# Performance work log

Measured on AMD Instinct MI355X. Metric: run time of the kernel, lower is better.

The kernel has to match this reference:

```python
import jax, jax.numpy as jnp
import numpy as np

EPS = 1e-8  # F.cosine_similarity eps
K = 2       # prompt_length


def setup_inputs() -> dict:
    key = jax.random.key(0)
    k1, k2, k3, k4 = jax.random.split(key, 4)
    B, DIM, NP, D = 32, 64, 4, 1024   # P: [batch, dim, N_p, D]; D == V (rows of stored table)
    E, VC = 768, 32000                 # stored table [V=D, E]; f_e: E -> vocab_dim=VC
    P = jax.random.normal(k1, (B, DIM, NP, D), dtype=jnp.float32)
    we_stored = jax.random.normal(k2, (D, E), dtype=jnp.float32) * 0.02
    fe_w = jax.random.normal(k3, (VC, E), dtype=jnp.float32) * 0.02
    fe_b = jax.random.normal(k4, (VC,), dtype=jnp.float32) * 0.02
    return {"P": P, "we_stored": we_stored, "fe_w": fe_w, "fe_b": fe_b}


def reference(P, we_stored, fe_w, fe_b):
    # word_embeddings = f_e(stored).t()  ->  [vocab_dim, V] == [VC, D]
    T = (we_stored @ fe_w.T + fe_b).T            # [VC, D]
    B, DIM, NP, D = P.shape
    # Cosine sim of each tiled embedding row (repeated N_p times) vs flattened P_i:
    #   dot(tiled_w, P_flat) = w . sum_j P[..., j, :]
    #   ||tiled_w|| = sqrt(N_p) * ||w||
    s = P.sum(axis=2)                                             # [B, DIM, D]
    w_norm = jnp.maximum(jnp.sqrt(jnp.float32(NP)) * jnp.linalg.norm(T, axis=1), EPS)   # [VC]
    p_norm = jnp.maximum(jnp.linalg.norm(P.reshape(B, DIM, -1), axis=-1), EPS)          # [B, DIM]
    scores = jnp.einsum('bdk,vk->bdv', s, T) / (w_norm[None, None, :] * p_norm[..., None])  # [B, DIM, VC]
    values, indices = jax.lax.top_k(scores, K)                    # [B, DIM, K]
    e_k = T[indices]                                              # [B, DIM, K, D]
    Z = jnp.concatenate([e_k, P], axis=2)                         # [B, DIM, NP+K, D]
    return Z, values
```

## Files before the change

### kernel.cpp

```cpp
#include <hip/hip_runtime.h>
#include <hip/hip_bf16.h>
#include <math.h>

#define B_    32
#define DIM_  64
#define NP_   4
#define D_    1024
#define E_    768
#define VC_   32000
#define R_    2048
#define KTOP  2
#define EPS_  1e-8f
#define NCB   250
#define NCAND 8

#define T_OFF    ((size_t)0)
#define TL_OFF   T_OFF
#define S_OFF    (T_OFF + (size_t)VC_ * D_)
#define INVW_OFF (S_OFF + (size_t)R_ * D_)
#define INVP_OFF (INVW_OFF + VC_)
#define WSQ_OFF  (INVP_OFF + R_)
#define PV_OFF   (WSQ_OFF + VC_)
#define PI_OFF   (PV_OFF + (size_t)R_ * NCB * 2)
#define SB_OFF   (PI_OFF + (size_t)R_ * NCB * 2)
#define TB_OFF   (SB_OFF + (size_t)R_ * D_ / 2)
#define WH_OFF   (TB_OFF + (size_t)VC_ * D_ / 2)
#define WL_OFF   (WH_OFF + (size_t)D_ * E_ / 2)
#define CAND_OFF (WL_OFF + (size_t)D_ * E_ / 2)
#define TIDX_OFF (CAND_OFF + (size_t)R_ * NCAND)
#define AH_OFF   (TIDX_OFF + (size_t)R_ * 2)
#define AL_OFF   (AH_OFF + (size_t)VC_ * E_ / 2)

#define NEG_INF (-3.4e38f)

typedef __bf16 bf16x8 __attribute__((ext_vector_type(8)));
typedef unsigned short u16x8 __attribute__((ext_vector_type(8)));
typedef float  f32x4  __attribute__((ext_vector_type(4)));

__device__ __forceinline__ void async_ld16(const void* gptr, void* lptr) {
    __builtin_amdgcn_global_load_lds(
        (const __attribute__((address_space(1))) void*)(uintptr_t)gptr,
        (__attribute__((address_space(3))) void*)(unsigned)(uintptr_t)lptr,
        16, 0, 0);
}

__device__ __forceinline__ bool better(float v, int i, float bv, int bi) {
    return (v > bv) || (v == bv && i < bi);
}

__device__ __forceinline__ float bfpair(unsigned short h, unsigned short l) {
    return __uint_as_float((unsigned)h << 16) + __uint_as_float((unsigned)l << 16);
}

__global__ __launch_bounds__(256) void k_prep_we(const float* __restrict__ x,
                                                 unsigned short* __restrict__ hi,
                                                 unsigned short* __restrict__ lo,
                                                 float* __restrict__ wsq) {
    int gi = blockIdx.x * 256 + threadIdx.x;
    if (gi < VC_) wsq[gi] = 0.f;
    int i = gi * 4;
    float4 v = *(const float4*)(x + i);
    ushort4 h, l;
    __bf16 b;
    b = (__bf16)v.x; h.x = __builtin_bit_cast(unsigned short, b); l.x = __builtin_bit_cast(unsigned short, (__bf16)(v.x - (float)b));
    b = (__bf16)v.y; h.y = __builtin_bit_cast(unsigned short, b); l.y = __builtin_bit_cast(unsigned short, (__bf16)(v.y - (float)b));
    b = (__bf16)v.z; h.z = __builtin_bit_cast(unsigned short, b); l.z = __builtin_bit_cast(unsigned short, (__bf16)(v.z - (float)b));
    b = (__bf16)v.w; h.w = __builtin_bit_cast(unsigned short, b); l.w = __builtin_bit_cast(unsigned short, (__bf16)(v.w - (float)b));
    *(ushort4*)(hi + i) = h;
    *(ushort4*)(lo + i) = l;
}

__global__ __launch_bounds__(256) void k_split(const float* __restrict__ x,
                                               unsigned short* __restrict__ hi,
                                               unsigned short* __restrict__ lo) {
    int i = (blockIdx.x * 256 + threadIdx.x) * 4;
    float4 v = *(const float4*)(x + i);
    ushort4 h, l;
    __bf16 b;
    b = (__bf16)v.x; h.x = __builtin_bit_cast(unsigned short, b); l.x = __builtin_bit_cast(unsigned short, (__bf16)(v.x - (float)b));
    b = (__bf16)v.y; h.y = __builtin_bit_cast(unsigned short, b); l.y = __builtin_bit_cast(unsigned short, (__bf16)(v.y - (float)b));
    b = (__bf16)v.z; h.z = __builtin_bit_cast(unsigned short, b); l.z = __builtin_bit_cast(unsigned short, (__bf16)(v.z - (float)b));
    b = (__bf16)v.w; h.w = __builtin_bit_cast(unsigned short, b); l.w = __builtin_bit_cast(unsigned short, (__bf16)(v.w - (float)b));
    *(ushort4*)(hi + i) = h;
    *(ushort4*)(lo + i) = l;
}

__global__ __launch_bounds__(256) void k_sum_pnorm(const float* __restrict__ P,
                                                   float* __restrict__ s,
                                                   unsigned short* __restrict__ sb,
                                                   float* __restrict__ invp,
                                                   float* __restrict__ outZ) {
    int r = blockIdx.x;
    int t = threadIdx.x;
    const float* base = P + (size_t)r * NP_ * D_;
    float4 acc = make_float4(0.f, 0.f, 0.f, 0.f);
    float sq = 0.f;
#pragma unroll
    for (int np = 0; np < NP_; ++np) {
        float4 v = *(const float4*)(base + (size_t)np * D_ + t * 4);
        acc.x += v.x; acc.y += v.y; acc.z += v.z; acc.w += v.w;
        sq += v.x * v.x + v.y * v.y + v.z * v.z + v.w * v.w;
        *(float4*)(outZ + ((size_t)r * 6 + KTOP + np) * D_ + t * 4) = v;
    }
    *(float4*)(s + (size_t)r * D_ + t * 4) = acc;
    ushort4 o;
    __bf16 b;
    b = (__bf16)acc.x; o.x = __builtin_bit_cast(unsigned short, b);
    b = (__bf16)acc.y; o.y = __builtin_bit_cast(unsigned short, b);
    b = (__bf16)acc.z; o.z = __builtin_bit_cast(unsigned short, b);
    b = (__bf16)acc.w; o.w = __builtin_bit_cast(unsigned short, b);
    *(ushort4*)(sb + (size_t)r * D_ + t * 4) = o;

    __shared__ float red[256];
    red[t] = sq;
    __syncthreads();
    for (int off = 128; off > 0; off >>= 1) {
        if (t < off) red[t] += red[t + off];
        __syncthreads();
    }
    if (t == 0) invp[r] = 1.0f / fmaxf(sqrtf(red[0]), EPS_);
}

__global__ __launch_bounds__(512) void k_gemm_T_mfma(const unsigned short* __restrict__ Ahg,
                                                     const unsigned short* __restrict__ Alg,
                                                     const unsigned short* __restrict__ Bhg,
                                                     const unsigned short* __restrict__ Blg,
                                                     const float* __restrict__ bias,
                                                     unsigned short* __restrict__ Th,
                                                     unsigned short* __restrict__ Tl,
                                                     float* __restrict__ wsq) {
    __shared__ __align__(16) unsigned short Ash[3][256 * 32];
    __shared__ __align__(16) unsigned short Asl[3][256 * 32];
    __shared__ __align__(16) unsigned short Bsh[3][128 * 32];
    __shared__ __align__(16) unsigned short Bsl[3][128 * 32];

    int tid = threadIdx.x;
    int wid = tid >> 6, lane = tid & 63;
    int quad = lane >> 4, l15 = lane & 15;
    int wm = wid >> 1, wn = wid & 1;
    int id  = blockIdx.x;
    int swz = (id & 7) * 125 + (id >> 3);
    int v0 = (swz >> 3) * 256;
    int d0 = (swz & 7) * 128;

    f32x4 acc[4][4];
#pragma unroll
    for (int i = 0; i < 4; ++i)
#pragma unroll
        for (int j = 0; j < 4; ++j) acc[i][j] = f32x4{0.f, 0.f, 0.f, 0.f};

    int r_lane = lane >> 2;
    int slot   = lane & 3;

#define STAGE_T(buf, kk)                                                           \
    {                                                                              \
_Pragma("unroll")                                                                  \
        for (int j = 0; j < 2; ++j) {                                              \
            int rowt = j * 128 + wid * 16 + r_lane;                                \
            int ss = (slot - (rowt >> 1)) & 3;                                     \
            async_ld16(Ahg + (size_t)(v0 + rowt) * E_ + (kk) + ss * 8,             \
                       (void*)(Ash[buf] + (j * 128 + wid * 16) * 32));             \
            async_ld16(Alg + (size_t)(v0 + rowt) * E_ + (kk) + ss * 8,             \
                       (void*)(Asl[buf] + (j * 128 + wid * 16) * 32));             \
        }                                                                          \
        {                                                                          \
            int rowb = wid * 16 + r_lane;                                          \
            int ssb = (slot - (rowb >> 1)) & 3;                                    \
            async_ld16(Bhg + (size_t)(d0 + rowb) * E_ + (kk) + ssb * 8,            \
                       (void*)(Bsh[buf] + (wid * 16) * 32));                       \
            async_ld16(Blg + (size_t)(d0 + rowb) * E_ + (kk) + ssb * 8,            \
                       (void*)(Bsl[buf] + (wid * 16) * 32));                       \
        }                                                                          \
    }

    STAGE_T(0, 0);
    STAGE_T(1, 32);

    const int NT = E_ / 32;
    int cur = 0;
    for (int kt = 0; kt < NT; ++kt) {
        int kn = (kt + 2 < NT) ? (kt + 2) * 32 : kt * 32;
        int nb = cur + 2; if (nb >= 3) nb -= 3;
        STAGE_T(nb, kn);

        asm volatile("s_waitcnt vmcnt(12)" ::: "memory");
        __builtin_amdgcn_s_barrier();
        asm volatile("" ::: "memory");

        bf16x8 fbh[4], fbl[4];
#pragma unroll
        for (int nt = 0; nt < 4; ++nt) {
            int row = wn * 64 + nt * 16 + l15;
            int ps = (quad + (row >> 1)) & 3;
            int off = row * 32 + ps * 8;
            fbh[nt] = *(const bf16x8*)(Bsh[cur] + off);
            fbl[nt] = *(const bf16x8*)(Bsl[cur] + off);
        }
        __builtin_amdgcn_s_setprio(1);
#pragma unroll
        for (int mt = 0; mt < 4; ++mt) {
            int row = wm * 64 + mt * 16 + l15;
            int ps = (quad + (row >> 1)) & 3;
            int off = row * 32 + ps * 8;
            bf16x8 fah = *(const bf16x8*)(Ash[cur] + off);
            bf16x8 fal = *(const bf16x8*)(Asl[cur] + off);
#pragma unroll
            for (int nt = 0; nt < 4; ++nt) {
                acc[mt][nt] = __builtin_amdgcn_mfma_f32_16x16x32_bf16(fah, fbh[nt], acc[mt][nt], 0, 0, 0);
                acc[mt][nt] = __builtin_amdgcn_mfma_f32_16x16x32_bf16(fal, fbh[nt], acc[mt][nt], 0, 0, 0);
                acc[mt][nt] = __builtin_amdgcn_mfma_f32_16x16x32_bf16(fah, fbl[nt], acc[mt][nt], 0, 0, 0);
            }
        }
        __builtin_amdgcn_s_setprio(0);

        __builtin_amdgcn_sched_barrier(0);
        __builtin_amdgcn_s_barrier();
        asm volatile("" ::: "memory");
        cur = (cur == 2) ? 0 : cur + 1;
    }
#undef STAGE_T

    float sq[4][4] = {};
#pragma unroll
    for (int mt = 0; mt < 4; ++mt) {
        int vbase = v0 + wm * 64 + mt * 16 + quad * 4;
        float bv[4];
#pragma unroll
        for (int rg = 0; rg < 4; ++rg) bv[rg] = bias[vbase + rg];
#pragma unroll
        for (int nt = 0; nt < 4; ++nt) {
            int d = d0 + wn * 64 + nt * 16 + l15;
#pragma unroll
            for (int rg = 0; rg < 4; ++rg) {
                float val = acc[mt][nt][rg] + bv[rg];
                __bf16 hb = (__bf16)val;
                __bf16 lb = (__bf16)(val - (float)hb);
                Th[(size_t)(vbase + rg) * D_ + d] = __builtin_bit_cast(unsigned short, hb);
                Tl[(size_t)(vbase + rg) * D_ + d] = __builtin_bit_cast(unsigned short, lb);
                sq[mt][rg] += val * val;
            }
        }
    }
#pragma unroll
    for (int mt = 0; mt < 4; ++mt)
#pragma unroll
        for (int rg = 0; rg < 4; ++rg) {
            float p = sq[mt][rg];
            p += __shfl_xor(p, 1); p += __shfl_xor(p, 2);
            p += __shfl_xor(p, 4); p += __shfl_xor(p, 8);
            if (l15 == 0) atomicAdd(&wsq[v0 + wm * 64 + mt * 16 + quad * 4 + rg], p);
        }
}

__global__ __launch_bounds__(256) void k_invw(const float* __restrict__ wsq,
                                              float* __restrict__ invw) {
    int v = blockIdx.x * 256 + threadIdx.x;
    if (v < VC_) invw[v] = 1.0f / fmaxf(2.0f * sqrtf(wsq[v]), EPS_);
}

__global__ __launch_bounds__(512) void k_scores_mfma(const unsigned short* __restrict__ Tb,
                                                     const unsigned short* __restrict__ sb,
                                                     const float* __restrict__ invw,
                                                     float* __restrict__ pval,
                                                     int* __restrict__ pidx) {
    __shared__ __align__(16) unsigned short As[4][256 * 32];
    __shared__ __align__(16) unsigned short Bs[4][256 * 32];

    int tid = threadIdx.x;
    int wid = tid >> 6, lane = tid & 63;
    int quad = lane >> 4, l15 = lane & 15;
    int wm = wid >> 2, wn = wid & 3;
    int id   = blockIdx.x;
    int swz  = (id & 7) * 125 + (id >> 3);
    int vblk = swz >> 3;
    int rblk = swz & 7;
    int v0 = vblk * 256;
    int r0 = rblk * 256;

    f32x4 acc[8][4];
#pragma unroll
    for (int i = 0; i < 8; ++i)
#pragma unroll
        for (int j = 0; j < 4; ++j) acc[i][j] = f32x4{0.f, 0.f, 0.f, 0.f};

    int r_lane = lane >> 2;
    int slot   = lane & 3;

#define STAGE_SC(buf, kk)                                                          \
    {                                                                              \
_Pragma("unroll")                                                                  \
        for (int j = 0; j < 2; ++j) {                                              \
            int rowt = j * 128 + wid * 16 + r_lane;                                \
            int ss = (slot - (rowt >> 1)) & 3;                                     \
            async_ld16(Tb + (size_t)(v0 + rowt) * D_ + (kk) + ss * 8,              \
                       (void*)(As[buf] + (j * 128 + wid * 16) * 32));              \
            async_ld16(sb + (size_t)(r0 + rowt) * D_ + (kk) + ss * 8,              \
                       (void*)(Bs[buf] + (j * 128 + wid * 16) * 32));              \
        }                                                                          \
    }

    STAGE_SC(0, 0);
    STAGE_SC(1, 32);
    STAGE_SC(2, 64);

    const int NT = D_ / 32;
    for (int kt = 0; kt < NT; ++kt) {
        int cur = kt & 3;
        int kn  = (kt + 3 < NT) ? (kt + 3) * 32 : kt * 32;
        STAGE_SC((kt + 3) & 3, kn);

        asm volatile("s_waitcnt vmcnt(12)" ::: "memory");
        __builtin_amdgcn_s_barrier();
        asm volatile("" ::: "memory");

        bf16x8 bfr[4];
#pragma unroll
        for (int nt = 0; nt < 4; ++nt) {
            int row = wn * 64 + nt * 16 + l15;
            int ps = (quad + (row >> 1)) & 3;
            bfr[nt] = *(const bf16x8*)(Bs[cur] + row * 32 + ps * 8);
        }
        __builtin_amdgcn_s_setprio(1);
#pragma unroll
        for (int mt = 0; mt < 8; ++mt) {
            int row = wm * 128 + mt * 16 + l15;
            int ps = (quad + (row >> 1)) & 3;
            bf16x8 af = *(const bf16x8*)(As[cur] + row * 32 + ps * 8);
#pragma unroll
            for (int nt = 0; nt < 4; ++nt)
                acc[mt][nt] = __builtin_amdgcn_mfma_f32_16x16x32_bf16(af, bfr[nt], acc[mt][nt], 0, 0, 0);
        }
        __builtin_amdgcn_s_setprio(0);

        __builtin_amdgcn_sched_barrier(0);
        __builtin_amdgcn_s_barrier();
        asm volatile("" ::: "memory");
    }
#undef STAGE_SC

    float iw[8][4];
#pragma unroll
    for (int mt = 0; mt < 8; ++mt)
#pragma unroll
        for (int rg = 0; rg < 4; ++rg)
            iw[mt][rg] = invw[v0 + wm * 128 + mt * 16 + quad * 4 + rg];

#pragma unroll
    for (int nt = 0; nt < 4; ++nt) {
        float b1 = NEG_INF, b2 = NEG_INF;
        int i1 = 0x7fffffff, i2 = 0x7fffffff;
#pragma unroll
        for (int mt = 0; mt < 8; ++mt)
#pragma unroll
            for (int rg = 0; rg < 4; ++rg) {
                float val = acc[mt][nt][rg] * iw[mt][rg];
                int v = v0 + wm * 128 + mt * 16 + quad * 4 + rg;
                if (better(val, v, b1, i1)) { b2 = b1; i2 = i1; b1 = val; i1 = v; }
                else if (better(val, v, b2, i2)) { b2 = val; i2 = v; }
            }
#pragma unroll
        for (int off = 16; off <= 32; off <<= 1) {
            float o1 = __shfl_xor(b1, off), o2 = __shfl_xor(b2, off);
            int  oi1 = __shfl_xor(i1, off), oi2 = __shfl_xor(i2, off);
            if (better(o1, oi1, b1, i1)) {
                if (better(b1, i1, o2, oi2)) { b2 = b1; i2 = i1; } else { b2 = o2; i2 = oi2; }
                b1 = o1; i1 = oi1;
            } else if (better(o1, oi1, b2, i2)) { b2 = o1; i2 = oi1; }
        }
        if (quad == 0) {
            int rl = wn * 64 + nt * 16 + l15;
            size_t off = ((size_t)(r0 + rl) * NCB + vblk * 2 + wm) * 2;
            pval[off] = b1;     pidx[off] = i1;
            pval[off + 1] = b2; pidx[off + 1] = i2;
        }
    }
}

__global__ __launch_bounds__(256) void k_topk8(const float* __restrict__ pval,
                                               const int* __restrict__ pidx,
                                               int* __restrict__ cands) {
    int r = blockIdx.x, t = threadIdx.x;
    __shared__ float v[512];
    __shared__ int  id[512];
    for (int c = t; c < 512; c += 256) {
        if (c < NCB * 2) { v[c] = pval[(size_t)r * NCB * 2 + c]; id[c] = pidx[(size_t)r * NCB * 2 + c]; }
        else             { v[c] = NEG_INF; id[c] = 0x7fffffff; }
    }
    __syncthreads();
    if (t == 0) {
        float bv[NCAND]; int bi[NCAND];
#pragma unroll
        for (int j = 0; j < NCAND; ++j) { bv[j] = NEG_INF; bi[j] = 0x7fffffff; }
        for (int c = 0; c < NCB * 2; ++c) {
            float x = v[c]; int xi = id[c];
            if (better(x, xi, bv[NCAND - 1], bi[NCAND - 1])) {
                int j = NCAND - 1;
                while (j > 0 && better(x, xi, bv[j - 1], bi[j - 1])) {
                    bv[j] = bv[j - 1]; bi[j] = bi[j - 1]; --j;
                }
                bv[j] = x; bi[j] = xi;
            }
        }
#pragma unroll
        for (int j = 0; j < NCAND; ++j) cands[r * NCAND + j] = bi[j];
    }
}

__global__ __launch_bounds__(256) void k_rescore(const float* __restrict__ s,
                                                 const unsigned short* __restrict__ Th,
                                                 const unsigned short* __restrict__ Tl,
                                                 const int* __restrict__ cands,
                                                 const float* __restrict__ invw,
                                                 const float* __restrict__ invp,
                                                 float* __restrict__ outv,
                                                 int* __restrict__ tidx) {
    int r = blockIdx.x, t = threadIdx.x;
    int cg = t >> 5, l32 = t & 31;
    int c = cands[r * NCAND + cg];
    const unsigned short* hrow = Th + (size_t)c * D_;
    const unsigned short* lrow = Tl + (size_t)c * D_;
    const float* srow = s + (size_t)r * D_;
    float p = 0.f;
#pragma unroll
    for (int j = 0; j < 8; ++j) {
        int e = (j * 32 + l32) * 4;
        float4 a = *(const float4*)(srow + e);
        ushort4 h = *(const ushort4*)(hrow + e);
        ushort4 l = *(const ushort4*)(lrow + e);
        p += a.x * bfpair(h.x, l.x) + a.y * bfpair(h.y, l.y)
           + a.z * bfpair(h.z, l.z) + a.w * bfpair(h.w, l.w);
    }
#pragma unroll
    for (int off = 16; off >= 1; off >>= 1) p += __shfl_xor(p, off);
    __shared__ float sc[NCAND];
    if (l32 == 0) sc[cg] = p;
    __syncthreads();
    if (t == 0) {
        float ip = invp[r];
        float b1 = NEG_INF, b2 = NEG_INF;
        int i1 = 0x7fffffff, i2 = 0x7fffffff;
#pragma unroll
        for (int j = 0; j < NCAND; ++j) {
            int ci = cands[r * NCAND + j];
            float val = sc[j] * invw[ci] * ip;
            if (better(val, ci, b1, i1)) { b2 = b1; i2 = i1; b1 = val; i1 = ci; }
            else if (better(val, ci, b2, i2)) { b2 = val; i2 = ci; }
        }
        outv[(size_t)r * 2 + 0] = b1;
        outv[(size_t)r * 2 + 1] = b2;
        tidx[r * 2 + 0] = i1;
        tidx[r * 2 + 1] = i2;
    }
}

__global__ __launch_bounds__(256) void k_writeZ(const unsigned short* __restrict__ Th,
                                                const unsigned short* __restrict__ Tl,
                                                const int* __restrict__ tidx,
                                                float* __restrict__ out) {
    int blk = blockIdx.x;
    int r = blk >> 1, j = blk & 1;
    size_t c = (size_t)tidx[r * 2 + j] * D_;
    int e = threadIdx.x * 4;
    ushort4 h = *(const ushort4*)(Th + c + e);
    ushort4 l = *(const ushort4*)(Tl + c + e);
    float4 v;
    v.x = bfpair(h.x, l.x); v.y = bfpair(h.y, l.y);
    v.z = bfpair(h.z, l.z); v.w = bfpair(h.w, l.w);
    *(float4*)(out + ((size_t)r * 6 + j) * D_ + e) = v;
}

extern "C" void kernel_launch(void* const* d_in, const int* in_sizes, int n_in,
                              void* d_out, int out_size, void* d_ws, size_t ws_size,
                              hipStream_t stream) {
    const float* P   = (const float*)d_in[0];
    const float* we  = (const float*)d_in[1];
    const float* few = (const float*)d_in[2];
    const float* feb = (const float*)d_in[3];
    float* out = (float*)d_out;
    float* ws  = (float*)d_ws;

    float* s    = ws + S_OFF;
    float* invw = ws + INVW_OFF;
    float* invp = ws + INVP_OFF;
    float* wsq  = ws + WSQ_OFF;
    float* pval = ws + PV_OFF;
    int*   pidx = (int*)(ws + PI_OFF);
    unsigned short* sb  = (unsigned short*)(ws + SB_OFF);
    unsigned short* Th  = (unsigned short*)(ws + TB_OFF);
    unsigned short* Tl  = (unsigned short*)(ws + TL_OFF);
    unsigned short* weh = (unsigned short*)(ws + WH_OFF);
    unsigned short* wel = (unsigned short*)(ws + WL_OFF);
    int*   cands = (int*)(ws + CAND_OFF);
    int*   tidx  = (int*)(ws + TIDX_OFF);
    unsigned short* fewh = (unsigned short*)(ws + AH_OFF);
    unsigned short* fewl = (unsigned short*)(ws + AL_OFF);
    float* outv = out + (size_t)R_ * 6 * D_;

    k_prep_we<<<(D_ * E_) / 1024, 256, 0, stream>>>(we, weh, wel, wsq);
    k_split<<<((size_t)VC_ * E_) / 1024, 256, 0, stream>>>(few, fewh, fewl);
    k_sum_pnorm<<<R_, 256, 0, stream>>>(P, s, sb, invp, out);
    k_gemm_T_mfma<<<1000, 512, 0, stream>>>(fewh, fewl, weh, wel, feb, Th, Tl, wsq);
    k_invw<<<(VC_ + 255) / 256, 256, 0, stream>>>(wsq, invw);
    k_scores_mfma<<<1000, 512, 0, stream>>>(Th, sb, invw, pval, pidx);
    k_topk8<<<R_, 256, 0, stream>>>(pval, pidx, cands);
    k_rescore<<<R_, 256, 0, stream>>>(s, Th, Tl, cands, invw, invp, outv, tidx);
    k_writeZ<<<R_ * 2, 256, 0, stream>>>(Th, Tl, tidx, out);
}
```

Baseline: 653.4 us.

## Fuse fe_w bf16 hi/lo split into T GEMM, loading fp32 tiles directly

Removes the separate k_split pass that converted the 32000x768 fe_w matrix into bf16 hi/lo arrays. The GEMM now async-loads fp32 A tiles into LDS with a rotated-slot swizzle and does the hi/lo split in registers before the MFMAs. This drops one full read plus two half-size writes and a re-read of the split arrays. In exchange it adds per-iteration conversion ALU work in the GEMM, raises A-tile LDS footprint (fp32 is the same bytes as hi+lo) and changes the bank-conflict pattern.

```diff
diff --git a/kernel.cpp b/kernel.cpp
--- a/kernel.cpp
+++ b/kernel.cpp
@@ -28,8 +28,6 @@
 #define WL_OFF   (WH_OFF + (size_t)D_ * E_ / 2)
 #define CAND_OFF (WL_OFF + (size_t)D_ * E_ / 2)
 #define TIDX_OFF (CAND_OFF + (size_t)R_ * NCAND)
-#define AH_OFF   (TIDX_OFF + (size_t)R_ * 2)
-#define AL_OFF   (AH_OFF + (size_t)VC_ * E_ / 2)
 
 #define NEG_INF (-3.4e38f)
 
@@ -70,21 +68,6 @@
     *(ushort4*)(lo + i) = l;
 }
 
-__global__ __launch_bounds__(256) void k_split(const float* __restrict__ x,
-                                               unsigned short* __restrict__ hi,
-                                               unsigned short* __restrict__ lo) {
-    int i = (blockIdx.x * 256 + threadIdx.x) * 4;
-    float4 v = *(const float4*)(x + i);
-    ushort4 h, l;
-    __bf16 b;
-    b = (__bf16)v.x; h.x = __builtin_bit_cast(unsigned short, b); l.x = __builtin_bit_cast(unsigned short, (__bf16)(v.x - (float)b));
-    b = (__bf16)v.y; h.y = __builtin_bit_cast(unsigned short, b); l.y = __builtin_bit_cast(unsigned short, (__bf16)(v.y - (float)b));
-    b = (__bf16)v.z; h.z = __builtin_bit_cast(unsigned short, b); l.z = __builtin_bit_cast(unsigned short, (__bf16)(v.z - (float)b));
-    b = (__bf16)v.w; h.w = __builtin_bit_cast(unsigned short, b); l.w = __builtin_bit_cast(unsigned short, (__bf16)(v.w - (float)b));
-    *(ushort4*)(hi + i) = h;
-    *(ushort4*)(lo + i) = l;
-}
-
 __global__ __launch_bounds__(256) void k_sum_pnorm(const float* __restrict__ P,
                                                    float* __restrict__ s,
                                                    unsigned short* __restrict__ sb,
@@ -121,16 +104,14 @@
     if (t == 0) invp[r] = 1.0f / fmaxf(sqrtf(red[0]), EPS_);
 }
 
-__global__ __launch_bounds__(512) void k_gemm_T_mfma(const unsigned short* __restrict__ Ahg,
-                                                     const unsigned short* __restrict__ Alg,
+__global__ __launch_bounds__(512) void k_gemm_T_mfma(const float* __restrict__ Afew,
                                                      const unsigned short* __restrict__ Bhg,
                                                      const unsigned short* __restrict__ Blg,
                                                      const float* __restrict__ bias,
                                                      unsigned short* __restrict__ Th,
                                                      unsigned short* __restrict__ Tl,
                                                      float* __restrict__ wsq) {
-    __shared__ __align__(16) unsigned short Ash[3][256 * 32];
-    __shared__ __align__(16) unsigned short Asl[3][256 * 32];
+    __shared__ __align__(16) float          Asf[3][256 * 32];
     __shared__ __align__(16) unsigned short Bsh[3][128 * 32];
     __shared__ __align__(16) unsigned short Bsl[3][128 * 32];
 
@@ -151,17 +132,17 @@
 
     int r_lane = lane >> 2;
     int slot   = lane & 3;
+    int ra_lane = lane >> 3;
+    int slota   = lane & 7;
 
 #define STAGE_T(buf, kk)                                                           \
     {                                                                              \
 _Pragma("unroll")                                                                  \
-        for (int j = 0; j < 2; ++j) {                                              \
-            int rowt = j * 128 + wid * 16 + r_lane;                                \
-            int ss = (slot - (rowt >> 1)) & 3;                                     \
-            async_ld16(Ahg + (size_t)(v0 + rowt) * E_ + (kk) + ss * 8,             \
-                       (void*)(Ash[buf] + (j * 128 + wid * 16) * 32));             \
-            async_ld16(Alg + (size_t)(v0 + rowt) * E_ + (kk) + ss * 8,             \
-                       (void*)(Asl[buf] + (j * 128 + wid * 16) * 32));             \
+        for (int j = 0; j < 4; ++j) {                                              \
+            int rowa = j * 64 + wid * 8 + ra_lane;                                 \
+            int ssa = (slota - (rowa & 7)) & 7;                                    \
+            async_ld16(Afew + (size_t)(v0 + rowa) * E_ + (kk) + ssa * 4,           \
+                       (void*)(Asf[buf] + (j * 64 + wid * 8) * 32));               \
         }                                                                          \
         {                                                                          \
             int rowb = wid * 16 + r_lane;                                          \
@@ -200,10 +181,21 @@
 #pragma unroll
         for (int mt = 0; mt < 4; ++mt) {
             int row = wm * 64 + mt * 16 + l15;
-            int ps = (quad + (row >> 1)) & 3;
-            int off = row * 32 + ps * 8;
-            bf16x8 fah = *(const bf16x8*)(Ash[cur] + off);
-            bf16x8 fal = *(const bf16x8*)(Asl[cur] + off);
+            int rot = row & 7;
+            const float* abase = Asf[cur] + row * 32;
+            int p1 = (2 * quad + rot) & 7;
+            int p2 = (2 * quad + 1 + rot) & 7;
+            f32x4 xa = *(const f32x4*)(abase + p1 * 4);
+            f32x4 xb = *(const f32x4*)(abase + p2 * 4);
+            bf16x8 fah, fal;
+#pragma unroll
+            for (int e = 0; e < 4; ++e) {
+                __bf16 h0 = (__bf16)xa[e];
+                __bf16 h1 = (__bf16)xb[e];
+                fah[e] = h0; fah[e + 4] = h1;
+                fal[e]     = (__bf16)(xa[e] - (float)h0);
+                fal[e + 4] = (__bf16)(xb[e] - (float)h1);
+            }
 #pragma unroll
             for (int nt = 0; nt < 4; ++nt) {
                 acc[mt][nt] = __builtin_amdgcn_mfma_f32_16x16x32_bf16(fah, fbh[nt], acc[mt][nt], 0, 0, 0);
@@ -492,14 +484,11 @@
     unsigned short* wel = (unsigned short*)(ws + WL_OFF);
     int*   cands = (int*)(ws + CAND_OFF);
     int*   tidx  = (int*)(ws + TIDX_OFF);
-    unsigned short* fewh = (unsigned short*)(ws + AH_OFF);
-    unsigned short* fewl = (unsigned short*)(ws + AL_OFF);
     float* outv = out + (size_t)R_ * 6 * D_;
 
     k_prep_we<<<(D_ * E_) / 1024, 256, 0, stream>>>(we, weh, wel, wsq);
-    k_split<<<((size_t)VC_ * E_) / 1024, 256, 0, stream>>>(few, fewh, fewl);
     k_sum_pnorm<<<R_, 256, 0, stream>>>(P, s, sb, invp, out);
-    k_gemm_T_mfma<<<1000, 512, 0, stream>>>(fewh, fewl, weh, wel, feb, Th, Tl, wsq);
+    k_gemm_T_mfma<<<1000, 512, 0, stream>>>(few, weh, wel, feb, Th, Tl, wsq);
     k_invw<<<(VC_ + 255) / 256, 256, 0, stream>>>(wsq, invw);
     k_scores_mfma<<<1000, 512, 0, stream>>>(Th, sb, invw, pval, pidx);
     k_topk8<<<R_, 256, 0, stream>>>(pval, pidx, cands);
```

Result: no change. 653.5 us (+0.0%).

## Fuse prep kernels, inline invw, and merge topk/rescore/writeZ into one kernel

Applied to the files above, without the earlier changes.

Merges the three preprocessing kernels into one launch that branches on block index. It drops the separate invw kernel by computing inverse norms from wsq inside the scores and final kernels. It also fuses top-8 candidate selection, fp32 rescoring and the Z gather into a single per-row kernel that keeps candidates in shared memory. This cuts the launch count from nine to four and removes several small global round trips, at the cost of a few redundant sqrt/div operations.

```diff
diff --git a/kernel.cpp b/kernel.cpp
--- a/kernel.cpp
+++ b/kernel.cpp
@@ -33,6 +33,11 @@
 
 #define NEG_INF (-3.4e38f)
 
+#define NB_WE   768
+#define NB_FEW  24000
+#define NB_SUM  R_
+#define NB_PREP (NB_WE + NB_FEW + NB_SUM)
+
 typedef __bf16 bf16x8 __attribute__((ext_vector_type(8)));
 typedef unsigned short u16x8 __attribute__((ext_vector_type(8)));
 typedef float  f32x4  __attribute__((ext_vector_type(4)));
@@ -52,13 +57,9 @@
     return __uint_as_float((unsigned)h << 16) + __uint_as_float((unsigned)l << 16);
 }
 
-__global__ __launch_bounds__(256) void k_prep_we(const float* __restrict__ x,
-                                                 unsigned short* __restrict__ hi,
-                                                 unsigned short* __restrict__ lo,
-                                                 float* __restrict__ wsq) {
-    int gi = blockIdx.x * 256 + threadIdx.x;
-    if (gi < VC_) wsq[gi] = 0.f;
-    int i = gi * 4;
+__device__ __forceinline__ void split4(const float* __restrict__ x, int i,
+                                       unsigned short* __restrict__ hi,
+                                       unsigned short* __restrict__ lo) {
     float4 v = *(const float4*)(x + i);
     ushort4 h, l;
     __bf16 b;
@@ -70,55 +71,57 @@
     *(ushort4*)(lo + i) = l;
 }
 
-__global__ __launch_bounds__(256) void k_split(const float* __restrict__ x,
-                                               unsigned short* __restrict__ hi,
-                                               unsigned short* __restrict__ lo) {
-    int i = (blockIdx.x * 256 + threadIdx.x) * 4;
-    float4 v = *(const float4*)(x + i);
-    ushort4 h, l;
-    __bf16 b;
-    b = (__bf16)v.x; h.x = __builtin_bit_cast(unsigned short, b); l.x = __builtin_bit_cast(unsigned short, (__bf16)(v.x - (float)b));
-    b = (__bf16)v.y; h.y = __builtin_bit_cast(unsigned short, b); l.y = __builtin_bit_cast(unsigned short, (__bf16)(v.y - (float)b));
-    b = (__bf16)v.z; h.z = __builtin_bit_cast(unsigned short, b); l.z = __builtin_bit_cast(unsigned short, (__bf16)(v.z - (float)b));
-    b = (__bf16)v.w; h.w = __builtin_bit_cast(unsigned short, b); l.w = __builtin_bit_cast(unsigned short, (__bf16)(v.w - (float)b));
-    *(ushort4*)(hi + i) = h;
-    *(ushort4*)(lo + i) = l;
-}
-
-__global__ __launch_bounds__(256) void k_sum_pnorm(const float* __restrict__ P,
-                                                   float* __restrict__ s,
-                                                   unsigned short* __restrict__ sb,
-                                                   float* __restrict__ invp,
-                                                   float* __restrict__ outZ) {
-    int r = blockIdx.x;
+__global__ __launch_bounds__(256) void k_prep(const float* __restrict__ we,
+                                              unsigned short* __restrict__ weh,
+                                              unsigned short* __restrict__ wel,
+                                              float* __restrict__ wsq,
+                                              const float* __restrict__ few,
+                                              unsigned short* __restrict__ fewh,
+                                              unsigned short* __restrict__ fewl,
+                                              const float* __restrict__ P,
+                                              float* __restrict__ s,
+                                              unsigned short* __restrict__ sb,
+                                              float* __restrict__ invp,
+                                              float* __restrict__ outZ) {
+    __shared__ float red[256];
+    int bid = blockIdx.x;
     int t = threadIdx.x;
-    const float* base = P + (size_t)r * NP_ * D_;
-    float4 acc = make_float4(0.f, 0.f, 0.f, 0.f);
-    float sq = 0.f;
-#pragma unroll
-    for (int np = 0; np < NP_; ++np) {
-        float4 v = *(const float4*)(base + (size_t)np * D_ + t * 4);
-        acc.x += v.x; acc.y += v.y; acc.z += v.z; acc.w += v.w;
-        sq += v.x * v.x + v.y * v.y + v.z * v.z + v.w * v.w;
-        *(float4*)(outZ + ((size_t)r * 6 + KTOP + np) * D_ + t * 4) = v;
-    }
-    *(float4*)(s + (size_t)r * D_ + t * 4) = acc;
-    ushort4 o;
-    __bf16 b;
-    b = (__bf16)acc.x; o.x = __builtin_bit_cast(unsigned short, b);
-    b = (__bf16)acc.y; o.y = __builtin_bit_cast(unsigned short, b);
-    b = (__bf16)acc.z; o.z = __builtin_bit_cast(unsigned short, b);
-    b = (__bf16)acc.w; o.w = __builtin_bit_cast(unsigned short, b);
-    *(ushort4*)(sb + (size_t)r * D_ + t * 4) = o;
-
-    __shared__ float red[256];
-    red[t] = sq;
-    __syncthreads();
-    for (int off = 128; off > 0; off >>= 1) {
-        if (t < off) red[t] += red[t + off];
+    if (bid < NB_WE) {
+        int gi = bid * 256 + t;
+        if (gi < VC_) wsq[gi] = 0.f;
+        split4(we, gi * 4, weh, wel);
+    } else if (bid < NB_WE + NB_FEW) {
+        int gi = (bid - NB_WE) * 256 + t;
+        split4(few, gi * 4, fewh, fewl);
+    } else {
+        int r = bid - (NB_WE + NB_FEW);
+        const float* base = P + (size_t)r * NP_ * D_;
+        float4 acc = make_float4(0.f, 0.f, 0.f, 0.f);
+        float sq = 0.f;
+#pragma unroll
+        for (int np = 0; np < NP_; ++np) {
+            float4 v = *(const float4*)(base + (size_t)np * D_ + t * 4);
+            acc.x += v.x; acc.y += v.y; acc.z += v.z; acc.w += v.w;
+            sq += v.x * v.x + v.y * v.y + v.z * v.z + v.w * v.w;
+            *(float4*)(outZ + ((size_t)r * 6 + KTOP + np) * D_ + t * 4) = v;
+        }
+        *(float4*)(s + (size_t)r * D_ + t * 4) = acc;
+        ushort4 o;
+        __bf16 b;
+        b = (__bf16)acc.x; o.x = __builtin_bit_cast(unsigned short, b);
+        b = (__bf16)acc.y; o.y = __builtin_bit_cast(unsigned short, b);
+        b = (__bf16)acc.z; o.z = __builtin_bit_cast(unsigned short, b);
+        b = (__bf16)acc.w; o.w = __builtin_bit_cast(unsigned short, b);
+        *(ushort4*)(sb + (size_t)r * D_ + t * 4) = o;
+
+        red[t] = sq;
         __syncthreads();
-    }
-    if (t == 0) invp[r] = 1.0f / fmaxf(sqrtf(red[0]), EPS_);
+        for (int off = 128; off > 0; off >>= 1) {
+            if (t < off) red[t] += red[t + off];
+            __syncthreads();
+        }
+        if (t == 0) invp[r] = 1.0f / fmaxf(sqrtf(red[0]), EPS_);
+    }
 }
 
 __global__ __launch_bounds__(512) void k_gemm_T_mfma(const unsigned short* __restrict__ Ahg,
@@ -252,15 +255,9 @@
         }
 }
 
-__global__ __launch_bounds__(256) void k_invw(const float* __restrict__ wsq,
-                                              float* __restrict__ invw) {
-    int v = blockIdx.x * 256 + threadIdx.x;
-    if (v < VC_) invw[v] = 1.0f / fmaxf(2.0f * sqrtf(wsq[v]), EPS_);
-}
-
 __global__ __launch_bounds__(512) void k_scores_mfma(const unsigned short* __restrict__ Tb,
                                                      const unsigned short* __restrict__ sb,
-                                                     const float* __restrict__ invw,
+                                                     const float* __restrict__ wsq,
                                                      float* __restrict__ pval,
                                                      int* __restrict__ pidx) {
     __shared__ __align__(16) unsigned short As[4][256 * 32];
@@ -342,8 +339,10 @@
 #pragma unroll
     for (int mt = 0; mt < 8; ++mt)
 #pragma unroll
-        for (int rg = 0; rg < 4; ++rg)
-            iw[mt][rg] = invw[v0 + wm * 128 + mt * 16 + quad * 4 + rg];
+        for (int rg = 0; rg < 4; ++rg) {
+            int v = v0 + wm * 128 + mt * 16 + quad * 4 + rg;
+            iw[mt][rg] = 1.0f / fmaxf(2.0f * sqrtf(wsq[v]), EPS_);
+        }
 
 #pragma unroll
     for (int nt = 0; nt < 4; ++nt) {
@@ -376,12 +375,22 @@
     }
 }
 
-__global__ __launch_bounds__(256) void k_topk8(const float* __restrict__ pval,
+__global__ __launch_bounds__(256) void k_final(const float* __restrict__ pval,
                                                const int* __restrict__ pidx,
-                                               int* __restrict__ cands) {
+                                               const float* __restrict__ s,
+                                               const unsigned short* __restrict__ Th,
+                                               const unsigned short* __restrict__ Tl,
+                                               const float* __restrict__ wsq,
+                                               const float* __restrict__ invp,
+                                               float* __restrict__ outv,
+                                               float* __restrict__ outZ) {
     int r = blockIdx.x, t = threadIdx.x;
     __shared__ float v[512];
     __shared__ int  id[512];
+    __shared__ int  cands[NCAND];
+    __shared__ float sc[NCAND];
+    __shared__ int  top2[2];
+
     for (int c = t; c < 512; c += 256) {
         if (c < NCB * 2) { v[c] = pval[(size_t)r * NCB * 2 + c]; id[c] = pidx[(size_t)r * NCB * 2 + c]; }
         else             { v[c] = NEG_INF; id[c] = 0x7fffffff; }
@@ -402,21 +411,12 @@
             }
         }
 #pragma unroll
-        for (int j = 0; j < NCAND; ++j) cands[r * NCAND + j] = bi[j];
-    }
-}
-
-__global__ __launch_bounds__(256) void k_rescore(const float* __restrict__ s,
-                                                 const unsigned short* __restrict__ Th,
-                                                 const unsigned short* __restrict__ Tl,
-                                                 const int* __restrict__ cands,
-                                                 const float* __restrict__ invw,
-                                                 const float* __restrict__ invp,
-                                                 float* __restrict__ outv,
-                                                 int* __restrict__ tidx) {
-    int r = blockIdx.x, t = threadIdx.x;
+        for (int j = 0; j < NCAND; ++j) cands[j] = bi[j];
+    }
+    __syncthreads();
+
     int cg = t >> 5, l32 = t & 31;
-    int c = cands[r * NCAND + cg];
+    int c = cands[cg];
     const unsigned short* hrow = Th + (size_t)c * D_;
     const unsigned short* lrow = Tl + (size_t)c * D_;
     const float* srow = s + (size_t)r * D_;
@@ -432,41 +432,37 @@
     }
 #pragma unroll
     for (int off = 16; off >= 1; off >>= 1) p += __shfl_xor(p, off);
-    __shared__ float sc[NCAND];
     if (l32 == 0) sc[cg] = p;
     __syncthreads();
+
     if (t == 0) {
         float ip = invp[r];
         float b1 = NEG_INF, b2 = NEG_INF;
         int i1 = 0x7fffffff, i2 = 0x7fffffff;
 #pragma unroll
         for (int j = 0; j < NCAND; ++j) {
-            int ci = cands[r * NCAND + j];
-            float val = sc[j] * invw[ci] * ip;
+            int ci = cands[j];
+            float val = sc[j] * (1.0f / fmaxf(2.0f * sqrtf(wsq[ci]), EPS_)) * ip;
             if (better(val, ci, b1, i1)) { b2 = b1; i2 = i1; b1 = val; i1 = ci; }
             else if (better(val, ci, b2, i2)) { b2 = val; i2 = ci; }
         }
         outv[(size_t)r * 2 + 0] = b1;
         outv[(size_t)r * 2 + 1] = b2;
-        tidx[r * 2 + 0] = i1;
-        tidx[r * 2 + 1] = i2;
-    }
-}
-
-__global__ __launch_bounds__(256) void k_writeZ(const unsigned short* __restrict__ Th,
-                                                const unsigned short* __restrict__ Tl,
-                                                const int* __restrict__ tidx,
-                                                float* __restrict__ out) {
-    int blk = blockIdx.x;
-    int r = blk >> 1, j = blk & 1;
-    size_t c = (size_t)tidx[r * 2 + j] * D_;
-    int e = threadIdx.x * 4;
-    ushort4 h = *(const ushort4*)(Th + c + e);
-    ushort4 l = *(const ushort4*)(Tl + c + e);
-    float4 v;
-    v.x = bfpair(h.x, l.x); v.y = bfpair(h.y, l.y);
-    v.z = bfpair(h.z, l.z); v.w = bfpair(h.w, l.w);
-    *(float4*)(out + ((size_t)r * 6 + j) * D_ + e) = v;
+        top2[0] = i1; top2[1] = i2;
+    }
+    __syncthreads();
+
+    int e = t * 4;
+#pragma unroll
+    for (int j = 0; j < 2; ++j) {
+        size_t cc = (size_t)top2[j] * D_;
+        ushort4 h = *(const ushort4*)(Th + cc + e);
+        ushort4 l = *(const ushort4*)(Tl + cc + e);
+        float4 z;
+        z.x = bfpair(h.x, l.x); z.y = bfpair(h.y, l.y);
+        z.z = bfpair(h.z, l.z); z.w = bfpair(h.w, l.w);
+        *(float4*)(outZ + ((size_t)r * 6 + j) * D_ + e) = z;
+    }
 }
 
 extern "C" void kernel_launch(void* const* d_in, const int* in_sizes, int n_in,
@@ -480,7 +476,6 @@
     float* ws  = (float*)d_ws;
 
     float* s    = ws + S_OFF;
-    float* invw = ws + INVW_OFF;
     float* invp = ws + INVP_OFF;
     float* wsq  = ws + WSQ_OFF;
     float* pval = ws + PV_OFF;
@@ -490,19 +485,13 @@
     unsigned short* Tl  = (unsigned short*)(ws + TL_OFF);
     unsigned short* weh = (unsigned short*)(ws + WH_OFF);
     unsigned short* wel = (unsigned short*)(ws + WL_OFF);
-    int*   cands = (int*)(ws + CAND_OFF);
-    int*   tidx  = (int*)(ws + TIDX_OFF);
     unsigned short* fewh = (unsigned short*)(ws + AH_OFF);
     unsigned short* fewl = (unsigned short*)(ws + AL_OFF);
     float* outv = out + (size_t)R_ * 6 * D_;
 
-    k_prep_we<<<(D_ * E_) / 1024, 256, 0, stream>>>(we, weh, wel, wsq);
-    k_split<<<((size_t)VC_ * E_) / 1024, 256, 0, stream>>>(few, fewh, fewl);
-    k_sum_pnorm<<<R_, 256, 0, stream>>>(P, s, sb, invp, out);
+    k_prep<<<NB_PREP, 256, 0, stream>>>(we, weh, wel, wsq, few, fewh, fewl,
+                                        P, s, sb, invp, out);
     k_gemm_T_mfma<<<1000, 512, 0, stream>>>(fewh, fewl, weh, wel, feb, Th, Tl, wsq);
-    k_invw<<<(VC_ + 255) / 256, 256, 0, stream>>>(wsq, invw);
-    k_scores_mfma<<<1000, 512, 0, stream>>>(Th, sb, invw, pval, pidx);
-    k_topk8<<<R_, 256, 0, stream>>>(pval, pidx, cands);
-    k_rescore<<<R_, 256, 0, stream>>>(s, Th, Tl, cands, invw, invp, outv, tidx);
-    k_writeZ<<<R_ * 2, 256, 0, stream>>>(Th, Tl, tidx, out);
-}
+    k_scores_mfma<<<1000, 512, 0, stream>>>(Th, sb, wsq, pval, pidx);
+    k_final<<<R_, 256, 0, stream>>>(pval, pidx, s, Th, Tl, wsq, invp, outv, out);
+}
```

Result: slower. 674.0 us (+3.2%).
